# Kernel optimization log

Measured on AMD Instinct MI355X. Metric: run time of the kernel, lower is better.

## Reference

```python
import jax, jax.numpy as jnp
import numpy as np

# B trajectories, L spline knots, D data channels, H hidden, W MLP width, OUT outputs
B, L, D, H, W, OUT = 1024, 200, 32, 64, 128, 16
N_STEPS = 100  # dt0 = (ts[-1]-ts[0]) / 100 in the source -> fixed-step Heun over the span


def _mlp3(x, W1, b1, W2, b2, W3, b3, act, final_act=None):
    h = act(x @ W1.T + b1)
    h = act(h @ W2.T + b2)
    o = h @ W3.T + b3
    return final_act(o) if final_act is not None else o


def setup_inputs() -> dict:
    key = jax.random.key(0)
    ks = jax.random.split(key, 16)
    f32 = jnp.float32

    def rn(k, shape, scale):
        return jax.random.normal(k, shape, f32) * scale

    def lin(kk, out_d, in_d):
        kw, kb = jax.random.split(kk)
        s = 1.0 / float(np.sqrt(in_d))
        return rn(kw, (out_d, in_d), s), rn(kb, (out_d,), s)

    inp = {"ts": jnp.arange(L, dtype=f32)}
    for i, n in enumerate(["coef_d", "coef_c", "coef_b", "coef_a"]):
        inp[n] = rn(ks[i], (B, L - 1, D), 0.1)
    inp["iW1"], inp["ib1"] = lin(ks[4], W, D)
    inp["iW2"], inp["ib2"] = lin(ks[5], W, W)
    inp["iW3"], inp["ib3"] = lin(ks[6], H, W)
    inp["fW1"], inp["fb1"] = lin(ks[7], W, H)
    inp["fW2"], inp["fb2"] = lin(ks[8], W, W)
    inp["fW3"], inp["fb3"] = lin(ks[9], H * D, W)
    inp["dW1"], inp["db1"] = lin(ks[10], 128, H)
    inp["dW2"], inp["db2"] = lin(ks[11], 128, 128)
    inp["dW3"], inp["db3"] = lin(ks[12], OUT, 128)
    return inp


def reference(ts, coef_d, coef_c, coef_b, coef_a,
              iW1, ib1, iW2, ib2, iW3, ib3,
              fW1, fb1, fW2, fb2, fW3, fb3,
              dW1, db1, dW2, db2, dW3, db3):
    sp = jax.nn.softplus
    # X(t0) = a[:, 0] (cubic-spline eval at left knot has frac = 0)
    y0 = _mlp3(coef_a[:, 0], iW1, ib1, iW2, ib2, iW3, ib3, sp, final_act=sp)  # [B, H]
    t0 = ts[0]
    dt = (ts[-1] - t0) / N_STEPS

    def dXdt(t):  # cubic spline derivative at scalar time t -> [B, D]
        i = jnp.clip(jnp.searchsorted(ts, t, side="right") - 1, 0, L - 2)
        frac = t - ts[i]
        return coef_b[:, i] + frac * (2.0 * coef_c[:, i] + 3.0 * frac * coef_d[:, i])

    def vf(t, y):  # ControlTerm(func, control).to_ode(): f(y) @ dX/dt
        f = _mlp3(y, fW1, fb1, fW2, fb2, fW3, fb3, sp).reshape(B, H, D)
        return jnp.einsum("bhd,bd->bh", f, dXdt(t))

    def heun_step(y, k):
        t = t0 + k * dt
        k1 = vf(t, y)
        k2 = vf(t + dt, y + dt * k1)
        return y + 0.5 * dt * (k1 + k2), None

    yT, _ = jax.lax.scan(heun_step, y0, jnp.arange(N_STEPS, dtype=ts.dtype))
    # decoder: Linear->relu->Linear->relu->Linear
    return _mlp3(yT, dW1, db1, dW2, db2, dW3, db3, jax.nn.relu)  # [B, OUT]
```

## Files before the change

### kernel.cpp

```cpp
#include <hip/hip_runtime.h>

#define NT 512
#define TRAJ 4

constexpr int Lk = 200;
constexpr int NSTEPS = 100;

__device__ __forceinline__ float sp_act(float x) {
    return fmaxf(x, 0.0f) + log1pf(expf(-fabsf(x)));
}

__global__ void fw3_transpose(const float* __restrict__ w, float* __restrict__ wT) {
    int idx = blockIdx.x * 256 + threadIdx.x;
    int k = idx >> 11;
    int n = idx & 2047;
    wT[idx] = w[n * 128 + k];
}

template<int O, int I>
__device__ __forceinline__ void stage_T(const float* __restrict__ g, float* __restrict__ T) {
    for (int base = threadIdx.x * 4; base < O * I; base += NT * 4) {
        const float4 w = *(const float4*)(g + base);
        const int o = base / I;
        const int i = base % I;
        T[(i + 0) * O + o] = w.x;
        T[(i + 1) * O + o] = w.y;
        T[(i + 2) * O + o] = w.z;
        T[(i + 3) * O + o] = w.w;
    }
}

template<int I, int O, int ACT>
__device__ __forceinline__ void mlp_layer(const float* __restrict__ T,
                                          const float* __restrict__ bias,
                                          const float* __restrict__ in, int inStride,
                                          float* __restrict__ out, int outStride) {
    const int tid = threadIdx.x;
    constexpr int TOT = TRAJ * O;
    for (int e = tid; e < TOT; e += NT) {
        const int t = e / O;
        const int o = e % O;
        const float* inr = in + t * inStride;
        float acc = bias[o];
        #pragma unroll 4
        for (int i = 0; i < I; ++i) acc = fmaf(inr[i], T[i * O + o], acc);
        if (ACT == 1) acc = sp_act(acc);
        else if (ACT == 2) acc = fmaxf(acc, 0.0f);
        out[t * outStride + o] = acc;
    }
}

__device__ __forceinline__ void evalvf(float t,
                                       const float* __restrict__ yin,
                                       float* __restrict__ kout,
                                       const float* __restrict__ wT1,
                                       const float* __restrict__ wT2,
                                       const float* __restrict__ fb1s,
                                       const float* __restrict__ fb2s,
                                       float* __restrict__ h1s,
                                       float* __restrict__ h2s,
                                       float* __restrict__ dXs,
                                       const float* __restrict__ ts,
                                       const float* __restrict__ coef_b,
                                       const float* __restrict__ coef_c,
                                       const float* __restrict__ coef_d,
                                       int bbase,
                                       const float4* __restrict__ wp,
                                       float4 fb3r)
{
    const int tid = threadIdx.x;

    if (tid < TRAJ * 32) {
        int i = (int)floorf(t);
        i = min(max(i, 0), Lk - 2);
        const float frac = t - ts[i];
        const int tt = tid >> 5, d = tid & 31;
        const size_t off = ((size_t)(bbase + tt) * 199 + (size_t)i) * 32 + d;
        dXs[tid] = coef_b[off] + frac * (2.0f * coef_c[off] + 3.0f * frac * coef_d[off]);
    }
    mlp_layer<64, 128, 1>(wT1, fb1s, yin, 64, h1s, 128);
    __syncthreads();
    mlp_layer<128, 128, 1>(wT2, fb2s, h1s, 128, h2s, 128);
    __syncthreads();

    float4 acc[TRAJ];
    #pragma unroll
    for (int t4 = 0; t4 < TRAJ; ++t4) acc[t4] = make_float4(0.f, 0.f, 0.f, 0.f);

    for (int k0 = 0; k0 < 128; k0 += 4) {
        const float4 w0 = wp[(k0 + 0) * 512];
        const float4 w1 = wp[(k0 + 1) * 512];
        const float4 w2 = wp[(k0 + 2) * 512];
        const float4 w3 = wp[(k0 + 3) * 512];
        #pragma unroll
        for (int t4 = 0; t4 < TRAJ; ++t4) {
            const float4 h = *(const float4*)(h2s + t4 * 128 + k0);
            float4 a = acc[t4];
            a.x = fmaf(h.x, w0.x, a.x); a.y = fmaf(h.x, w0.y, a.y); a.z = fmaf(h.x, w0.z, a.z); a.w = fmaf(h.x, w0.w, a.w);
            a.x = fmaf(h.y, w1.x, a.x); a.y = fmaf(h.y, w1.y, a.y); a.z = fmaf(h.y, w1.z, a.z); a.w = fmaf(h.y, w1.w, a.w);
            a.x = fmaf(h.z, w2.x, a.x); a.y = fmaf(h.z, w2.y, a.y); a.z = fmaf(h.z, w2.z, a.z); a.w = fmaf(h.z, w2.w, a.w);
            a.x = fmaf(h.w, w3.x, a.x); a.y = fmaf(h.w, w3.y, a.y); a.z = fmaf(h.w, w3.z, a.z); a.w = fmaf(h.w, w3.w, a.w);
            acc[t4] = a;
        }
    }

    const int dbase = 4 * (tid & 7);
    float part[TRAJ];
    #pragma unroll
    for (int t4 = 0; t4 < TRAJ; ++t4) {
        const float4 dx = *(const float4*)(dXs + t4 * 32 + dbase);
        part[t4] = (acc[t4].x + fb3r.x) * dx.x + (acc[t4].y + fb3r.y) * dx.y +
                   (acc[t4].z + fb3r.z) * dx.z + (acc[t4].w + fb3r.w) * dx.w;
    }
    #pragma unroll
    for (int m = 1; m < 8; m <<= 1) {
        #pragma unroll
        for (int t4 = 0; t4 < TRAJ; ++t4) part[t4] += __shfl_xor(part[t4], m, 64);
    }
    if ((tid & 7) == 0) {
        const int h = tid >> 3;
        #pragma unroll
        for (int t4 = 0; t4 < TRAJ; ++t4) kout[t4 * 64 + h] = part[t4];
    }
    __syncthreads();
}

__global__ __launch_bounds__(NT, 1)
void cde_kernel(const float* __restrict__ ts,
                const float* __restrict__ coef_d, const float* __restrict__ coef_c,
                const float* __restrict__ coef_b, const float* __restrict__ coef_a,
                const float* __restrict__ iW1, const float* __restrict__ ib1,
                const float* __restrict__ iW2, const float* __restrict__ ib2,
                const float* __restrict__ iW3, const float* __restrict__ ib3,
                const float* __restrict__ fW1, const float* __restrict__ fb1,
                const float* __restrict__ fW2, const float* __restrict__ fb2,
                const float* __restrict__ fb3,
                const float* __restrict__ dW1, const float* __restrict__ db1,
                const float* __restrict__ dW2, const float* __restrict__ db2,
                const float* __restrict__ dW3, const float* __restrict__ db3,
                const float* __restrict__ fW3T,
                float* __restrict__ outp)
{
    __shared__ float wreg[28672];
    __shared__ float h1s[TRAJ * 128], h2s[TRAJ * 128];
    __shared__ float ys[TRAJ * 64], ys2[TRAJ * 64], k1s[TRAJ * 64], k2s[TRAJ * 64];
    __shared__ float dXs[TRAJ * 32], a0s[TRAJ * 32];
    __shared__ float fb1s[128], fb2s[128];

    const int tid = threadIdx.x;
    const int bbase = blockIdx.x * TRAJ;

    const float ts0 = ts[0];
    const float dt = (ts[Lk - 1] - ts0) / (float)NSTEPS;
    const float4 fb3r = *((const float4*)fb3 + tid);
    const float4* wp = (const float4*)fW3T + tid;

    if (tid < TRAJ * 32) {
        const int t = tid >> 5, d = tid & 31;
        a0s[t * 32 + d] = coef_a[((size_t)(bbase + t) * 199) * 32 + d];
    }
    stage_T<128, 32>(iW1, wreg);
    stage_T<128, 128>(iW2, wreg + 32 * 128);
    stage_T<64, 128>(iW3, wreg + 32 * 128 + 128 * 128);
    if (tid < 128) { fb1s[tid] = fb1[tid]; fb2s[tid] = fb2[tid]; }
    __syncthreads();
    mlp_layer<32, 128, 1>(wreg, ib1, a0s, 32, h1s, 128);
    __syncthreads();
    mlp_layer<128, 128, 1>(wreg + 32 * 128, ib2, h1s, 128, h2s, 128);
    __syncthreads();
    mlp_layer<128, 64, 1>(wreg + 32 * 128 + 128 * 128, ib3, h2s, 128, ys, 64);
    __syncthreads();

    stage_T<128, 64>(fW1, wreg);
    stage_T<128, 128>(fW2, wreg + 64 * 128);
    __syncthreads();

    for (int step = 0; step < NSTEPS; ++step) {
        const float t1 = ts0 + (float)step * dt;
        evalvf(t1, ys, k1s, wreg, wreg + 64 * 128, fb1s, fb2s, h1s, h2s, dXs,
               ts, coef_b, coef_c, coef_d, bbase, wp, fb3r);
        if (tid < TRAJ * 64) ys2[tid] = ys[tid] + dt * k1s[tid];
        __syncthreads();
        evalvf(t1 + dt, ys2, k2s, wreg, wreg + 64 * 128, fb1s, fb2s, h1s, h2s, dXs,
               ts, coef_b, coef_c, coef_d, bbase, wp, fb3r);
        if (tid < TRAJ * 64) ys[tid] += 0.5f * dt * (k1s[tid] + k2s[tid]);
        __syncthreads();
    }

    stage_T<128, 64>(dW1, wreg);
    stage_T<128, 128>(dW2, wreg + 64 * 128);
    stage_T<16, 128>(dW3, wreg + 64 * 128 + 128 * 128);
    __syncthreads();
    mlp_layer<64, 128, 2>(wreg, db1, ys, 64, h1s, 128);
    __syncthreads();
    mlp_layer<128, 128, 2>(wreg + 64 * 128, db2, h1s, 128, h2s, 128);
    __syncthreads();
    mlp_layer<128, 16, 0>(wreg + 64 * 128 + 128 * 128, db3, h2s, 128,
                          outp + (size_t)bbase * 16, 16);
}

extern "C" void kernel_launch(void* const* d_in, const int* in_sizes, int n_in,
                              void* d_out, int out_size, void* d_ws, size_t ws_size,
                              hipStream_t stream) {
    (void)in_sizes; (void)n_in; (void)out_size; (void)ws_size;
    const float* ts     = (const float*)d_in[0];
    const float* coef_d = (const float*)d_in[1];
    const float* coef_c = (const float*)d_in[2];
    const float* coef_b = (const float*)d_in[3];
    const float* coef_a = (const float*)d_in[4];
    const float* iW1 = (const float*)d_in[5];  const float* ib1 = (const float*)d_in[6];
    const float* iW2 = (const float*)d_in[7];  const float* ib2 = (const float*)d_in[8];
    const float* iW3 = (const float*)d_in[9];  const float* ib3 = (const float*)d_in[10];
    const float* fW1 = (const float*)d_in[11]; const float* fb1 = (const float*)d_in[12];
    const float* fW2 = (const float*)d_in[13]; const float* fb2 = (const float*)d_in[14];
    const float* fW3 = (const float*)d_in[15]; const float* fb3 = (const float*)d_in[16];
    const float* dW1 = (const float*)d_in[17]; const float* db1 = (const float*)d_in[18];
    const float* dW2 = (const float*)d_in[19]; const float* db2 = (const float*)d_in[20];
    const float* dW3 = (const float*)d_in[21]; const float* db3 = (const float*)d_in[22];

    float* fW3T = (float*)d_ws;

    fw3_transpose<<<1024, 256, 0, stream>>>(fW3, fW3T);
    cde_kernel<<<256, NT, 0, stream>>>(ts, coef_d, coef_c, coef_b, coef_a,
                                       iW1, ib1, iW2, ib2, iW3, ib3,
                                       fW1, fb1, fW2, fb2, fb3,
                                       dW1, db1, dW2, db2, dW3, db3,
                                       fW3T, (float*)d_out);
}
```

Measured before the change: 2.685 ms.

## Pack weights to bf16, halve trajectories per block, use packed FMA

The fW3 weights and the 128x128 layer weights are converted to bf16 and packed in pairs, which halves LDS and global traffic for the big matmuls and lets the shared footprint fit several blocks per CU. TRAJ drops from 4 to 2 and the grid doubles to 512 blocks, with launch bounds raised to allow 4 blocks per CU. Inner loops use two-wide float vector FMAs. The Heun loop is flattened into one loop of 200 vector-field evaluations with the state update fused into the reduction, removing some barriers. The cost is reduced weight precision (bf16 rounding), which may exceed the tolerance, and fewer trajectories share each weight load.

```diff
diff --git a/kernel.cpp b/kernel.cpp
--- a/kernel.cpp
+++ b/kernel.cpp
@@ -1,20 +1,48 @@
 #include <hip/hip_runtime.h>
 
 #define NT 512
-#define TRAJ 4
+#define TRAJ 2
 
 constexpr int Lk = 200;
 constexpr int NSTEPS = 100;
 
+typedef float f32x2 __attribute__((ext_vector_type(2)));
+
+#if __has_builtin(__builtin_elementwise_fma)
+#define FMA2(a, b, c) __builtin_elementwise_fma((a), (b), (c))
+#else
+static __device__ __forceinline__ f32x2 fma2_(f32x2 a, f32x2 b, f32x2 c) {
+    c.x = fmaf(a.x, b.x, c.x); c.y = fmaf(a.y, b.y, c.y); return c;
+}
+#define FMA2 fma2_
+#endif
+
 __device__ __forceinline__ float sp_act(float x) {
     return fmaxf(x, 0.0f) + log1pf(expf(-fabsf(x)));
 }
 
-__global__ void fw3_transpose(const float* __restrict__ w, float* __restrict__ wT) {
-    int idx = blockIdx.x * 256 + threadIdx.x;
-    int k = idx >> 11;
-    int n = idx & 2047;
-    wT[idx] = w[n * 128 + k];
+__device__ __forceinline__ unsigned int f2bf(float f) {
+    union { float f; unsigned int u; } v; v.f = f;
+    unsigned int u = v.u + 0x7FFFu + ((v.u >> 16) & 1u);
+    return u >> 16;
+}
+__device__ __forceinline__ float bflo(unsigned int u) { return __uint_as_float(u << 16); }
+__device__ __forceinline__ float bfhi(unsigned int u) { return __uint_as_float(u & 0xFFFF0000u); }
+
+__global__ void fw3_packbf(const float* __restrict__ w, uint4* __restrict__ p) {
+    const int s = blockIdx.x * 256 + threadIdx.x;
+    const int town = s & 511;
+    const int c = s >> 9;
+    const int j = c & 3, ko = c >> 2;
+    const int n = 4 * town + j;
+    const float4 a = *(const float4*)(w + n * 128 + ko * 8);
+    const float4 b = *(const float4*)(w + n * 128 + ko * 8 + 4);
+    uint4 o;
+    o.x = f2bf(a.x) | (f2bf(a.y) << 16);
+    o.y = f2bf(a.z) | (f2bf(a.w) << 16);
+    o.z = f2bf(b.x) | (f2bf(b.y) << 16);
+    o.w = f2bf(b.z) | (f2bf(b.w) << 16);
+    p[s] = o;
 }
 
 template<int O, int I>
@@ -27,6 +55,16 @@
         T[(i + 1) * O + o] = w.y;
         T[(i + 2) * O + o] = w.z;
         T[(i + 3) * O + o] = w.w;
+    }
+}
+
+template<int O, int I>
+__device__ __forceinline__ void stage_Tp(const float* __restrict__ g, unsigned int* __restrict__ Tp) {
+    for (int base = threadIdx.x * 2; base < O * I; base += NT * 2) {
+        const float2 w = *(const float2*)(g + base);
+        const int o = base / I;
+        const int i = base % I;
+        Tp[(i >> 1) * O + o] = f2bf(w.x) | (f2bf(w.y) << 16);
     }
 }
 
@@ -41,91 +79,48 @@
         const int t = e / O;
         const int o = e % O;
         const float* inr = in + t * inStride;
-        float acc = bias[o];
+        f32x2 a2; a2.x = bias[o]; a2.y = 0.0f;
         #pragma unroll 4
-        for (int i = 0; i < I; ++i) acc = fmaf(inr[i], T[i * O + o], acc);
+        for (int i = 0; i < I; i += 2) {
+            f32x2 xv; xv.x = inr[i];        xv.y = inr[i + 1];
+            f32x2 wv; wv.x = T[i * O + o];  wv.y = T[(i + 1) * O + o];
+            a2 = FMA2(xv, wv, a2);
+        }
+        float acc = a2.x + a2.y;
         if (ACT == 1) acc = sp_act(acc);
         else if (ACT == 2) acc = fmaxf(acc, 0.0f);
         out[t * outStride + o] = acc;
     }
 }
 
-__device__ __forceinline__ void evalvf(float t,
-                                       const float* __restrict__ yin,
-                                       float* __restrict__ kout,
-                                       const float* __restrict__ wT1,
-                                       const float* __restrict__ wT2,
-                                       const float* __restrict__ fb1s,
-                                       const float* __restrict__ fb2s,
-                                       float* __restrict__ h1s,
-                                       float* __restrict__ h2s,
-                                       float* __restrict__ dXs,
-                                       const float* __restrict__ ts,
-                                       const float* __restrict__ coef_b,
-                                       const float* __restrict__ coef_c,
-                                       const float* __restrict__ coef_d,
-                                       int bbase,
-                                       const float4* __restrict__ wp,
-                                       float4 fb3r)
-{
+template<int I, int O, int ACT, int OMAJOR>
+__device__ __forceinline__ void mlp_layer_p(const unsigned int* __restrict__ Tp,
+                                            const float* __restrict__ bias,
+                                            const float* __restrict__ in, int inStride,
+                                            float* __restrict__ out, int outStride) {
     const int tid = threadIdx.x;
-
-    if (tid < TRAJ * 32) {
-        int i = (int)floorf(t);
-        i = min(max(i, 0), Lk - 2);
-        const float frac = t - ts[i];
-        const int tt = tid >> 5, d = tid & 31;
-        const size_t off = ((size_t)(bbase + tt) * 199 + (size_t)i) * 32 + d;
-        dXs[tid] = coef_b[off] + frac * (2.0f * coef_c[off] + 3.0f * frac * coef_d[off]);
-    }
-    mlp_layer<64, 128, 1>(wT1, fb1s, yin, 64, h1s, 128);
-    __syncthreads();
-    mlp_layer<128, 128, 1>(wT2, fb2s, h1s, 128, h2s, 128);
-    __syncthreads();
-
-    float4 acc[TRAJ];
-    #pragma unroll
-    for (int t4 = 0; t4 < TRAJ; ++t4) acc[t4] = make_float4(0.f, 0.f, 0.f, 0.f);
-
-    for (int k0 = 0; k0 < 128; k0 += 4) {
-        const float4 w0 = wp[(k0 + 0) * 512];
-        const float4 w1 = wp[(k0 + 1) * 512];
-        const float4 w2 = wp[(k0 + 2) * 512];
-        const float4 w3 = wp[(k0 + 3) * 512];
-        #pragma unroll
-        for (int t4 = 0; t4 < TRAJ; ++t4) {
-            const float4 h = *(const float4*)(h2s + t4 * 128 + k0);
-            float4 a = acc[t4];
-            a.x = fmaf(h.x, w0.x, a.x); a.y = fmaf(h.x, w0.y, a.y); a.z = fmaf(h.x, w0.z, a.z); a.w = fmaf(h.x, w0.w, a.w);
-            a.x = fmaf(h.y, w1.x, a.x); a.y = fmaf(h.y, w1.y, a.y); a.z = fmaf(h.y, w1.z, a.z); a.w = fmaf(h.y, w1.w, a.w);
-            a.x = fmaf(h.z, w2.x, a.x); a.y = fmaf(h.z, w2.y, a.y); a.z = fmaf(h.z, w2.z, a.z); a.w = fmaf(h.z, w2.w, a.w);
-            a.x = fmaf(h.w, w3.x, a.x); a.y = fmaf(h.w, w3.y, a.y); a.z = fmaf(h.w, w3.z, a.z); a.w = fmaf(h.w, w3.w, a.w);
-            acc[t4] = a;
-        }
-    }
-
-    const int dbase = 4 * (tid & 7);
-    float part[TRAJ];
-    #pragma unroll
-    for (int t4 = 0; t4 < TRAJ; ++t4) {
-        const float4 dx = *(const float4*)(dXs + t4 * 32 + dbase);
-        part[t4] = (acc[t4].x + fb3r.x) * dx.x + (acc[t4].y + fb3r.y) * dx.y +
-                   (acc[t4].z + fb3r.z) * dx.z + (acc[t4].w + fb3r.w) * dx.w;
-    }
-    #pragma unroll
-    for (int m = 1; m < 8; m <<= 1) {
-        #pragma unroll
-        for (int t4 = 0; t4 < TRAJ; ++t4) part[t4] += __shfl_xor(part[t4], m, 64);
-    }
-    if ((tid & 7) == 0) {
-        const int h = tid >> 3;
-        #pragma unroll
-        for (int t4 = 0; t4 < TRAJ; ++t4) kout[t4 * 64 + h] = part[t4];
-    }
-    __syncthreads();
-}
-
-__global__ __launch_bounds__(NT, 1)
+    constexpr int TOT = TRAJ * O;
+    for (int e = tid; e < TOT; e += NT) {
+        const int t = e / O;
+        const int o = e % O;
+        const float* inr = in + t * inStride;
+        f32x2 a2; a2.x = bias[o]; a2.y = 0.0f;
+        #pragma unroll 4
+        for (int ip = 0; ip < I / 2; ++ip) {
+            const unsigned int u = Tp[ip * O + o];
+            f32x2 xv = *(const f32x2*)(inr + 2 * ip);
+            f32x2 wv; wv.x = bflo(u); wv.y = bfhi(u);
+            a2 = FMA2(xv, wv, a2);
+        }
+        float acc = a2.x + a2.y;
+        if (ACT == 1) acc = sp_act(acc);
+        else if (ACT == 2) acc = fmaxf(acc, 0.0f);
+        if (OMAJOR) out[o * TRAJ + t] = acc;
+        else        out[t * outStride + o] = acc;
+    }
+}
+
+__global__ __launch_bounds__(NT, 4)
 void cde_kernel(const float* __restrict__ ts,
                 const float* __restrict__ coef_d, const float* __restrict__ coef_c,
                 const float* __restrict__ coef_b, const float* __restrict__ coef_a,
@@ -138,65 +133,139 @@
                 const float* __restrict__ dW1, const float* __restrict__ db1,
                 const float* __restrict__ dW2, const float* __restrict__ db2,
                 const float* __restrict__ dW3, const float* __restrict__ db3,
-                const float* __restrict__ fW3T,
+                const uint4* __restrict__ fW3B,
                 float* __restrict__ outp)
 {
-    __shared__ float wreg[28672];
-    __shared__ float h1s[TRAJ * 128], h2s[TRAJ * 128];
-    __shared__ float ys[TRAJ * 64], ys2[TRAJ * 64], k1s[TRAJ * 64], k2s[TRAJ * 64];
-    __shared__ float dXs[TRAJ * 32], a0s[TRAJ * 32];
-    __shared__ float fb1s[128], fb2s[128];
+    __shared__ __align__(16) float R[17408];
+    __shared__ __align__(16) float h1s[TRAJ * 128];
+    __shared__ __align__(16) float hbuf[TRAJ * 128];
+    __shared__ __align__(16) float h2T[128 * TRAJ];
+    __shared__ __align__(16) float ys[TRAJ * 64], ys2[TRAJ * 64], k1s[TRAJ * 64];
+    __shared__ __align__(16) float dXsT[32 * TRAJ];
+    __shared__ __align__(16) float a0s[TRAJ * 32];
+    __shared__ __align__(16) float fb1s[128], fb2s[128];
 
     const int tid = threadIdx.x;
     const int bbase = blockIdx.x * TRAJ;
 
     const float ts0 = ts[0];
     const float dt = (ts[Lk - 1] - ts0) / (float)NSTEPS;
+    const float hdt = 0.5f * dt;
     const float4 fb3r = *((const float4*)fb3 + tid);
-    const float4* wp = (const float4*)fW3T + tid;
+    const uint4* wq = fW3B + tid;
 
     if (tid < TRAJ * 32) {
         const int t = tid >> 5, d = tid & 31;
         a0s[t * 32 + d] = coef_a[((size_t)(bbase + t) * 199) * 32 + d];
     }
-    stage_T<128, 32>(iW1, wreg);
-    stage_T<128, 128>(iW2, wreg + 32 * 128);
-    stage_T<64, 128>(iW3, wreg + 32 * 128 + 128 * 128);
+    stage_T<128, 32>(iW1, R);
+    stage_Tp<128, 128>(iW2, (unsigned int*)(R + 4096));
+    stage_Tp<64, 128>(iW3, (unsigned int*)(R + 12288));
     if (tid < 128) { fb1s[tid] = fb1[tid]; fb2s[tid] = fb2[tid]; }
     __syncthreads();
-    mlp_layer<32, 128, 1>(wreg, ib1, a0s, 32, h1s, 128);
-    __syncthreads();
-    mlp_layer<128, 128, 1>(wreg + 32 * 128, ib2, h1s, 128, h2s, 128);
-    __syncthreads();
-    mlp_layer<128, 64, 1>(wreg + 32 * 128 + 128 * 128, ib3, h2s, 128, ys, 64);
-    __syncthreads();
-
-    stage_T<128, 64>(fW1, wreg);
-    stage_T<128, 128>(fW2, wreg + 64 * 128);
-    __syncthreads();
-
-    for (int step = 0; step < NSTEPS; ++step) {
-        const float t1 = ts0 + (float)step * dt;
-        evalvf(t1, ys, k1s, wreg, wreg + 64 * 128, fb1s, fb2s, h1s, h2s, dXs,
-               ts, coef_b, coef_c, coef_d, bbase, wp, fb3r);
-        if (tid < TRAJ * 64) ys2[tid] = ys[tid] + dt * k1s[tid];
+    mlp_layer<32, 128, 1>(R, ib1, a0s, 32, h1s, 128);
+    __syncthreads();
+    mlp_layer_p<128, 128, 1, 0>((unsigned int*)(R + 4096), ib2, h1s, 128, hbuf, 128);
+    __syncthreads();
+    mlp_layer_p<128, 64, 1, 0>((unsigned int*)(R + 12288), ib3, hbuf, 128, ys, 64);
+    __syncthreads();
+
+    stage_T<128, 64>(fW1, R);
+    stage_Tp<128, 128>(fW2, (unsigned int*)(R + 8192));
+    __syncthreads();
+
+    #pragma unroll 1
+    for (int e = 0; e < 2 * NSTEPS; ++e) {
+        const bool k2e = e & 1;
+        const float t1 = ts0 + (float)(e >> 1) * dt + (k2e ? dt : 0.0f);
+        const float* yin  = k2e ? ys2 : ys;
+        float*       yout = k2e ? ys  : ys2;
+
+        if (tid < TRAJ * 32) {
+            int i = (int)floorf(t1);
+            i = min(max(i, 0), Lk - 2);
+            const float frac = t1 - ts[i];
+            const int t = tid >> 5, d = tid & 31;
+            const size_t off = ((size_t)(bbase + t) * 199 + (size_t)i) * 32 + d;
+            dXsT[d * TRAJ + t] = coef_b[off] + frac * (2.0f * coef_c[off] + 3.0f * frac * coef_d[off]);
+        }
+
+        mlp_layer<64, 128, 1>(R, fb1s, yin, 64, h1s, 128);
         __syncthreads();
-        evalvf(t1 + dt, ys2, k2s, wreg, wreg + 64 * 128, fb1s, fb2s, h1s, h2s, dXs,
-               ts, coef_b, coef_c, coef_d, bbase, wp, fb3r);
-        if (tid < TRAJ * 64) ys[tid] += 0.5f * dt * (k1s[tid] + k2s[tid]);
+        mlp_layer_p<128, 128, 1, 1>((unsigned int*)(R + 8192), fb2s, h1s, 128, h2T, TRAJ);
         __syncthreads();
-    }
-
-    stage_T<128, 64>(dW1, wreg);
-    stage_T<128, 128>(dW2, wreg + 64 * 128);
-    stage_T<16, 128>(dW3, wreg + 64 * 128 + 128 * 128);
-    __syncthreads();
-    mlp_layer<64, 128, 2>(wreg, db1, ys, 64, h1s, 128);
-    __syncthreads();
-    mlp_layer<128, 128, 2>(wreg + 64 * 128, db2, h1s, 128, h2s, 128);
-    __syncthreads();
-    mlp_layer<128, 16, 0>(wreg + 64 * 128 + 128 * 128, db3, h2s, 128,
-                          outp + (size_t)bbase * 16, 16);
+
+        f32x2 acc0, acc1, acc2, acc3;
+        acc0.x = acc0.y = fb3r.x;
+        acc1.x = acc1.y = fb3r.y;
+        acc2.x = acc2.y = fb3r.z;
+        acc3.x = acc3.y = fb3r.w;
+
+        #pragma unroll 2
+        for (int ko = 0; ko < 16; ++ko) {
+            const uint4 u0 = wq[(ko * 4 + 0) * 512];
+            const uint4 u1 = wq[(ko * 4 + 1) * 512];
+            const uint4 u2 = wq[(ko * 4 + 2) * 512];
+            const uint4 u3 = wq[(ko * 4 + 3) * 512];
+            const float* hp = h2T + ko * 8 * TRAJ;
+            f32x2 h[8];
+            #pragma unroll
+            for (int q = 0; q < 8; ++q) h[q] = *(const f32x2*)(hp + q * TRAJ);
+            #pragma unroll
+            for (int q = 0; q < 4; ++q) {
+                const unsigned int w0 = (q == 0) ? u0.x : (q == 1) ? u0.y : (q == 2) ? u0.z : u0.w;
+                const unsigned int w1 = (q == 0) ? u1.x : (q == 1) ? u1.y : (q == 2) ? u1.z : u1.w;
+                const unsigned int w2 = (q == 0) ? u2.x : (q == 1) ? u2.y : (q == 2) ? u2.z : u2.w;
+                const unsigned int w3 = (q == 0) ? u3.x : (q == 1) ? u3.y : (q == 2) ? u3.z : u3.w;
+                f32x2 s;
+                s.x = s.y = bflo(w0); acc0 = FMA2(h[2 * q], s, acc0);
+                s.x = s.y = bfhi(w0); acc0 = FMA2(h[2 * q + 1], s, acc0);
+                s.x = s.y = bflo(w1); acc1 = FMA2(h[2 * q], s, acc1);
+                s.x = s.y = bfhi(w1); acc1 = FMA2(h[2 * q + 1], s, acc1);
+                s.x = s.y = bflo(w2); acc2 = FMA2(h[2 * q], s, acc2);
+                s.x = s.y = bfhi(w2); acc2 = FMA2(h[2 * q + 1], s, acc2);
+                s.x = s.y = bflo(w3); acc3 = FMA2(h[2 * q], s, acc3);
+                s.x = s.y = bfhi(w3); acc3 = FMA2(h[2 * q + 1], s, acc3);
+            }
+        }
+
+        const int dj = 4 * (tid & 7);
+        f32x2 part; part.x = part.y = 0.0f;
+        part = FMA2(acc0, *(const f32x2*)(dXsT + (dj + 0) * TRAJ), part);
+        part = FMA2(acc1, *(const f32x2*)(dXsT + (dj + 1) * TRAJ), part);
+        part = FMA2(acc2, *(const f32x2*)(dXsT + (dj + 2) * TRAJ), part);
+        part = FMA2(acc3, *(const f32x2*)(dXsT + (dj + 3) * TRAJ), part);
+
+        float px = part.x, py = part.y;
+        #pragma unroll
+        for (int m = 1; m < 8; m <<= 1) {
+            px += __shfl_xor(px, m, 64);
+            py += __shfl_xor(py, m, 64);
+        }
+
+        if ((tid & 7) == 0) {
+            const int h = tid >> 3;
+            if (!k2e) {
+                k1s[h] = px;      yout[h]      = ys[h]      + dt * px;
+                k1s[64 + h] = py; yout[64 + h] = ys[64 + h] + dt * py;
+            } else {
+                yout[h]      = ys[h]      + hdt * (k1s[h] + px);
+                yout[64 + h] = ys[64 + h] + hdt * (k1s[64 + h] + py);
+            }
+        }
+        __syncthreads();
+    }
+
+    stage_T<128, 64>(dW1, R);
+    stage_Tp<128, 128>(dW2, (unsigned int*)(R + 8192));
+    stage_Tp<16, 128>(dW3, (unsigned int*)(R + 16384));
+    __syncthreads();
+    mlp_layer<64, 128, 2>(R, db1, ys, 64, h1s, 128);
+    __syncthreads();
+    mlp_layer_p<128, 128, 2, 0>((unsigned int*)(R + 8192), db2, h1s, 128, hbuf, 128);
+    __syncthreads();
+    mlp_layer_p<128, 16, 0, 0>((unsigned int*)(R + 16384), db3, hbuf, 128,
+                               outp + (size_t)bbase * 16, 16);
 }
 
 extern "C" void kernel_launch(void* const* d_in, const int* in_sizes, int n_in,
@@ -218,12 +287,12 @@
     const float* dW2 = (const float*)d_in[19]; const float* db2 = (const float*)d_in[20];
     const float* dW3 = (const float*)d_in[21]; const float* db3 = (const float*)d_in[22];
 
-    float* fW3T = (float*)d_ws;
-
-    fw3_transpose<<<1024, 256, 0, stream>>>(fW3, fW3T);
-    cde_kernel<<<256, NT, 0, stream>>>(ts, coef_d, coef_c, coef_b, coef_a,
+    uint4* fW3B = (uint4*)d_ws;
+
+    fw3_packbf<<<128, 256, 0, stream>>>(fW3, fW3B);
+    cde_kernel<<<512, NT, 0, stream>>>(ts, coef_d, coef_c, coef_b, coef_a,
                                        iW1, ib1, iW2, ib2, iW3, ib3,
                                        fW1, fb1, fW2, fb2, fb3,
                                        dW1, db1, dW2, db2, dW3, db3,
-                                       fW3T, (float*)d_out);
-}
+                                       fW3B, (float*)d_out);
+}
```

New measurement: 2.960 ms. +10.3%, slower.
